# Performance work log

Hardware: AMD Instinct MI355X
Metric: run time of the kernel (lower is better)

Reference implementation:

```python
import jax, jax.numpy as jnp
import numpy as np
from jax import lax

B, C, H, W = 8, 384, 32, 32
HEADS, GROUPS = 12, 3
CG = C // GROUPS          # 128 channels per offset group
HD = C // HEADS           # 32 head dim
NS = H * W                # sampled kv points (one per query location)
EPS = 1e-5


def setup_inputs() -> dict:
    key = jax.random.key(0)
    ks = jax.random.split(key, 10)
    w = lambda k, sh, sc=0.02: (jax.random.normal(k, sh, jnp.float32) * sc)
    return {
        "x1": jax.random.normal(ks[0], (B, C, H, W), jnp.float32),
        "x2": jax.random.normal(ks[1], (B, C, H, W), jnp.float32),
        "Wq": w(ks[2], (C, C)), "bq": jnp.zeros((C,), jnp.float32),
        "Wk": w(ks[3], (C, C)), "bk": jnp.zeros((C,), jnp.float32),
        "Wv": w(ks[4], (C, C)), "bv": jnp.zeros((C,), jnp.float32),
        "Wo": w(ks[5], (C, C)), "bo": jnp.zeros((C,), jnp.float32),
        "off_dw": w(ks[6], (CG, 1, 5, 5)),       # depthwise 5x5 offset conv
        "off_dw_b": jnp.zeros((CG,), jnp.float32),
        "ln_g": jnp.ones((CG,), jnp.float32),
        "ln_b": jnp.zeros((CG,), jnp.float32),
        "off_w": w(ks[7], (2, CG), 0.01),         # 1x1 conv -> 2 offset channels
    }


def _conv1x1(x, Wm, bm):
    return jnp.einsum('oc,bchw->bohw', Wm, x) + bm[None, :, None, None]


def _ref_grid():
    # normalized reference points in [-1,1], channel 0 = x (width), 1 = y (height)
    xs = (jnp.arange(W, dtype=jnp.float32) + 0.5) / W * 2.0 - 1.0
    ys = (jnp.arange(H, dtype=jnp.float32) + 0.5) / H * 2.0 - 1.0
    gy, gx = jnp.meshgrid(ys, xs, indexing='ij')   # [H,W]
    return jnp.stack([gx, gy], axis=0)             # [2,H,W]


def _forward(x1, x2, Wq, bq, Wk, bk, Wv, bv, Wo, bo,
             off_dw, off_dw_b, ln_g, ln_b, off_w):
    BG = B * GROUPS
    q = _conv1x1(x1, Wq, bq)                                   # [B,C,H,W]

    # --- offset network (per group) ---
    qg = q.reshape(BG, CG, H, W)
    t = lax.conv_general_dilated(qg, off_dw, (1, 1), 'SAME',
                                 dimension_numbers=('NCHW', 'OIHW', 'NCHW'),
                                 feature_group_count=CG)
    t = t + off_dw_b[None, :, None, None]
    mu = jnp.mean(t, axis=1, keepdims=True)
    var = jnp.var(t, axis=1, keepdims=True)
    t = (t - mu) * lax.rsqrt(var + EPS)
    t = t * ln_g[None, :, None, None] + ln_b[None, :, None, None]
    t = jax.nn.gelu(t)
    off = jnp.einsum('oc,bchw->bohw', off_w, t)                # [BG,2,H,W]

    pos = jnp.clip(off + _ref_grid()[None], -1.0, 1.0)         # [BG,2,H,W]
    px = pos[:, 0].reshape(BG, NS)
    py = pos[:, 1].reshape(BG, NS)

    # --- bilinear grid_sample of x2 (align_corners=True) ---
    ix = (px + 1.0) * 0.5 * (W - 1)
    iy = (py + 1.0) * 0.5 * (H - 1)
    x0f, y0f = jnp.floor(ix), jnp.floor(iy)
    wx, wy = ix - x0f, iy - y0f
    x0 = jnp.clip(x0f.astype(jnp.int32), 0, W - 1)
    x1i = jnp.clip(x0 + 1, 0, W - 1)
    y0 = jnp.clip(y0f.astype(jnp.int32), 0, H - 1)
    y1i = jnp.clip(y0 + 1, 0, H - 1)

    x2g = x2.reshape(BG, CG, H * W)

    def gather(yi, xi):
        idx = yi * W + xi                                      # [BG,NS]
        idx = jnp.broadcast_to(idx[:, None, :], (BG, CG, NS))
        return jnp.take_along_axis(x2g, idx, axis=2)           # [BG,CG,NS]

    v00, v01 = gather(y0, x0), gather(y0, x1i)
    v10, v11 = gather(y1i, x0), gather(y1i, x1i)
    wx_, wy_ = wx[:, None, :], wy[:, None, :]
    samp = (v00 * (1 - wx_) * (1 - wy_) + v01 * wx_ * (1 - wy_)
            + v10 * (1 - wx_) * wy_ + v11 * wx_ * wy_)         # [BG,CG,NS]
    samp = samp.reshape(B, C, NS)

    # --- multi-head attention between q and sampled k/v ---
    k = jnp.einsum('oc,bcn->bon', Wk, samp) + bk[None, :, None]
    v = jnp.einsum('oc,bcn->bon', Wv, samp) + bv[None, :, None]
    qf = q.reshape(B, HEADS, HD, NS)
    kf = k.reshape(B, HEADS, HD, NS)
    vf = v.reshape(B, HEADS, HD, NS)
    scale = 1.0 / np.sqrt(HD).astype(np.float32)
    attn = jax.nn.softmax(jnp.einsum('bhdq,bhdk->bhqk', qf * scale, kf), axis=-1)
    out = jnp.einsum('bhqk,bhdk->bhdq', attn, vf).reshape(B, C, H, W)
    y = _conv1x1(out, Wo, bo)
    return x1 + y                                              # residual add (drop_path=0 -> Identity)


def reference(x1, x2, Wq, bq, Wk, bk, Wv, bv, Wo, bo,
              off_dw, off_dw_b, ln_g, ln_b, off_w):
    return _forward(x1, x2, Wq, bq, Wk, bk, Wv, bv, Wo, bo,
                    off_dw, off_dw_b, ln_g, ln_b, off_w)
```

## Files before the change

kernel.cpp:

```cpp
#include <hip/hip_runtime.h>
#include <math.h>

#define B_  8
#define C_  384
#define NS_ 1024
#define HEADS_ 12
#define HD_ 32
#define GROUPS_ 3
#define CG_ 128
#define EPS_ 1e-5f
#define QSC2 (0.17677669529663687f * 1.4426950408889634f)

typedef __attribute__((ext_vector_type(8))) short bf16x8;
typedef __attribute__((ext_vector_type(4))) short bf16x4;
typedef __attribute__((ext_vector_type(4))) float f32x4;
typedef __attribute__((ext_vector_type(8))) __bf16 b8;

static __device__ __forceinline__ short f2b(float f) {
  union { float f; unsigned u; } v; v.f = f;
  unsigned r = v.u + 0x7fffu + ((v.u >> 16) & 1u);
  return (short)(r >> 16);
}
static __device__ __forceinline__ float b2f(short s) {
  union { unsigned u; float f; } v; v.u = ((unsigned)(unsigned short)s) << 16;
  return v.f;
}

#if __has_builtin(__builtin_amdgcn_exp2f)
#define EXP2(x) __builtin_amdgcn_exp2f(x)
#else
#define EXP2(x) exp2f(x)
#endif

static __device__ __forceinline__ unsigned cvtpk(float lo, float hi) {
  unsigned r;
  asm("v_cvt_pk_bf16_f32 %0, %1, %2" : "=v"(r) : "v"(lo), "v"(hi));
  return r;
}

static __device__ __forceinline__ f32x4 MFMA(bf16x8 a, bf16x8 b, f32x4 c) {
  return __builtin_amdgcn_mfma_f32_16x16x32_bf16(
      __builtin_bit_cast(b8, a), __builtin_bit_cast(b8, b), c, 0, 0, 0);
}

__global__ void convw(const float* __restrict__ s0, const float* __restrict__ s1,
                      const float* __restrict__ s2, const float* __restrict__ s3,
                      short* __restrict__ d0, short* __restrict__ d1,
                      short* __restrict__ d2, short* __restrict__ d3, int n) {
  int i = blockIdx.x * 256 + threadIdx.x;
  if (i >= n) return;
  const float* s = blockIdx.y == 0 ? s0 : blockIdx.y == 1 ? s1 : blockIdx.y == 2 ? s2 : s3;
  short*       d = blockIdx.y == 0 ? d0 : blockIdx.y == 1 ? d1 : blockIdx.y == 2 ? d2 : d3;
  d[i] = f2b(s[i]);
}

__global__ void convdw(const float* __restrict__ dw, float* __restrict__ dwp) {
  int i = blockIdx.x * 256 + threadIdx.x;
  if (i < 25 * CG_) {
    int t = i / CG_, c = i % CG_;
    dwp[i] = dw[c * 25 + t];
  }
}

template <int CH>
__global__ __launch_bounds__(256) void transp(const float* __restrict__ src,
                                              short* __restrict__ dst) {
  __shared__ float tl[32][33];
  int n0 = blockIdx.x * 32, c0 = blockIdx.y * 32, b = blockIdx.z;
  int tx = threadIdx.x & 31, ty = threadIdx.x >> 5;
#pragma unroll
  for (int i = 0; i < 4; ++i)
    tl[ty + 8 * i][tx] = src[((size_t)b * CH + c0 + ty + 8 * i) * NS_ + n0 + tx];
  __syncthreads();
#pragma unroll
  for (int i = 0; i < 4; ++i)
    dst[((size_t)b * NS_ + n0 + ty + 8 * i) * CH + c0 + tx] = f2b(tl[tx][ty + 8 * i]);
}

#define GLOADA(kc_, AF)                                                        \
  _Pragma("unroll")                                                            \
  for (int rt = 0; rt < 4; ++rt)                                               \
    AF[rt] = *(const bf16x8*)(Ab + (size_t)(n0 + wr + rt * 16 + r15) * C_ +    \
                              (kc_) + g * 8);
#define GLOADB(kc_, BF, WP, MOFF)                                              \
  _Pragma("unroll")                                                            \
  for (int ct = 0; ct < 4; ++ct)                                               \
    BF[ct] = *(const bf16x8*)((WP) + (size_t)((MOFF) + ct * 16 + r15) * C_ +   \
                              (kc_) + g * 8);
#define GMFMA(AF, BF)                                                          \
  _Pragma("unroll")                                                            \
  for (int rt = 0; rt < 4; ++rt)                                               \
    _Pragma("unroll")                                                          \
    for (int ct = 0; ct < 4; ++ct) acc[rt][ct] = MFMA(AF[rt], BF[ct], acc[rt][ct]);

template <int MODE>
__global__ __launch_bounds__(256) void gemm_nm(
    const short* __restrict__ A, const short* __restrict__ Wb,
    const float* __restrict__ bias, const float* __restrict__ res,
    short* __restrict__ outb, float* __restrict__ outf) {
  int b = blockIdx.z;
  int n0 = blockIdx.x * 128;
  int m0 = blockIdx.y * 128;
  int wv = threadIdx.x >> 6;
  int lane = threadIdx.x & 63;
  int g = lane >> 4, r15 = lane & 15;
  int wr = (wv >> 1) * 64, wc = (wv & 1) * 64;

  const short* Ab = A + (size_t)b * NS_ * C_;
  f32x4 acc[4][4];
#pragma unroll
  for (int i = 0; i < 4; ++i)
#pragma unroll
    for (int j = 0; j < 4; ++j) acc[i][j] = (f32x4){0.f, 0.f, 0.f, 0.f};

  bf16x8 afA[4], bfA[4], afB[4], bfB[4];
  GLOADA(0, afA); GLOADB(0, bfA, Wb, m0 + wc);
#pragma unroll
  for (int cp = 0; cp < 6; ++cp) {
    GLOADA(64 * cp + 32, afB); GLOADB(64 * cp + 32, bfB, Wb, m0 + wc);
    GMFMA(afA, bfA);
    if (cp < 5) { GLOADA(64 * cp + 64, afA); GLOADB(64 * cp + 64, bfA, Wb, m0 + wc); }
    GMFMA(afB, bfB);
  }

#pragma unroll
  for (int rt = 0; rt < 4; ++rt)
#pragma unroll
    for (int ct = 0; ct < 4; ++ct) {
      int m = m0 + wc + ct * 16 + r15;
      int nb = n0 + wr + rt * 16 + g * 4;
      float bv = bias[m];
      f32x4 v = acc[rt][ct];
      v.x += bv; v.y += bv; v.z += bv; v.w += bv;
      if (MODE == 1) {
        *(f32x4*)(outf + ((size_t)b * C_ + m) * NS_ + nb) = v;
        outb[((size_t)b * NS_ + nb + 0) * C_ + m] = f2b(v.x * QSC2);
        outb[((size_t)b * NS_ + nb + 1) * C_ + m] = f2b(v.y * QSC2);
        outb[((size_t)b * NS_ + nb + 2) * C_ + m] = f2b(v.z * QSC2);
        outb[((size_t)b * NS_ + nb + 3) * C_ + m] = f2b(v.w * QSC2);
      } else {
        const f32x4 rv = *(const f32x4*)(res + ((size_t)b * C_ + m) * NS_ + nb);
        v.x += rv.x; v.y += rv.y; v.z += rv.z; v.w += rv.w;
        *(f32x4*)(outf + ((size_t)b * C_ + m) * NS_ + nb) = v;
      }
    }
}

__global__ __launch_bounds__(256) void gemm_kv(
    const short* __restrict__ A, const short* __restrict__ Wkb,
    const short* __restrict__ Wvb, const float* __restrict__ bkv,
    const float* __restrict__ bvv, short* __restrict__ kblk,
    short* __restrict__ vblk) {
  int b = blockIdx.z;
  int n0 = blockIdx.x * 128;
  int m0 = blockIdx.y * 64;
  int wv = threadIdx.x >> 6;
  int lane = threadIdx.x & 63;
  int g = lane >> 4, r15 = lane & 15;
  int wr = (wv >> 1) * 64;
  int isv = wv & 1;
  const short* Wsel = isv ? Wvb : Wkb;
  const float* bsel = isv ? bvv : bkv;

  const short* Ab = A + (size_t)b * NS_ * C_;
  f32x4 acc[4][4];
#pragma unroll
  for (int i = 0; i < 4; ++i)
#pragma unroll
    for (int j = 0; j < 4; ++j) acc[i][j] = (f32x4){0.f, 0.f, 0.f, 0.f};

  bf16x8 afA[4], bfA[4], afB[4], bfB[4];
  GLOADA(0, afA); GLOADB(0, bfA, Wsel, m0);
#pragma unroll
  for (int cp = 0; cp < 6; ++cp) {
    GLOADA(64 * cp + 32, afB); GLOADB(64 * cp + 32, bfB, Wsel, m0);
    GMFMA(afA, bfA);
    if (cp < 5) { GLOADA(64 * cp + 64, afA); GLOADB(64 * cp + 64, bfA, Wsel, m0); }
    GMFMA(afB, bfB);
  }

#pragma unroll
  for (int rt = 0; rt < 4; ++rt)
#pragma unroll
    for (int ct = 0; ct < 4; ++ct) {
      int m = m0 + ct * 16 + r15;
      int nb = n0 + wr + rt * 16 + g * 4;
      float bv = bsel[m];
      f32x4 v = acc[rt][ct];
      v.x += bv; v.y += bv; v.z += bv; v.w += bv;
      int h = m >> 5, dh = m & 31;
      if (!isv) {
        size_t hb = ((size_t)(b * HEADS_ + h) * 32 + (nb >> 5)) * 1024 +
                    (((nb >> 4) & 1) ? 512 : 0);
        int base_l = (nb & 15) | ((dh >> 3) << 4);
        int jj = dh & 7;
        kblk[hb + (size_t)(base_l + 0) * 8 + jj] = f2b(v.x);
        kblk[hb + (size_t)(base_l + 1) * 8 + jj] = f2b(v.y);
        kblk[hb + (size_t)(base_l + 2) * 8 + jj] = f2b(v.z);
        kblk[hb + (size_t)(base_l + 3) * 8 + jj] = f2b(v.w);
      } else {
        int dt = dh >> 4, q15v = dh & 15;
        int kk = nb & 31;
        int half = kk >> 4, gk = (kk & 15) >> 2;
        size_t off = ((size_t)(b * HEADS_ + h) * 32 + (nb >> 5)) * 1024 +
                     dt * 512 + (size_t)((q15v | (gk << 4))) * 8 + half * 4;
        bf16x4 s4 = {f2b(v.x), f2b(v.y), f2b(v.z), f2b(v.w)};
        *(bf16x4*)(vblk + off) = s4;
      }
    }
}

__global__ __launch_bounds__(256) void offsample4(
    const float* __restrict__ qd,
    const short* __restrict__ x2t,
    const float* __restrict__ dwp,
    const float* __restrict__ dwb,
    const float* __restrict__ lng, const float* __restrict__ lnb,
    const float* __restrict__ offw, short* __restrict__ samp) {
  int bg = blockIdx.x, y = blockIdx.y;
  int tid = threadIdx.x;
  int xg = tid >> 5, cc = tid & 31;
  int x0 = xg << 2, c0 = cc << 2;

  const float* qb = qd + ((size_t)bg * CG_ + c0) * NS_;

  f32x4 dwb4 = *(const f32x4*)(dwb + c0);
  float a[4][4];
#pragma unroll
  for (int i = 0; i < 4; ++i)
#pragma unroll
    for (int p = 0; p < 4; ++p) a[i][p] = dwb4[i];

#pragma unroll
  for (int dy = -2; dy <= 2; ++dy) {
    int yy = y + dy;
    if (yy < 0 || yy > 31) continue;
    f32x4 w0 = *(const f32x4*)(dwp + ((dy + 2) * 5 + 0) * CG_ + c0);
    f32x4 w1 = *(const f32x4*)(dwp + ((dy + 2) * 5 + 1) * CG_ + c0);
    f32x4 w2 = *(const f32x4*)(dwp + ((dy + 2) * 5 + 2) * CG_ + c0);
    f32x4 w3 = *(const f32x4*)(dwp + ((dy + 2) * 5 + 3) * CG_ + c0);
    f32x4 w4 = *(const f32x4*)(dwp + ((dy + 2) * 5 + 4) * CG_ + c0);
#pragma unroll
    for (int i = 0; i < 4; ++i) {
      const float* row = qb + (size_t)i * NS_ + yy * 32;
      f32x4 wa = (f32x4){0.f, 0.f, 0.f, 0.f};
      f32x4 wcv = (f32x4){0.f, 0.f, 0.f, 0.f};
      if (x0 >= 4)  wa  = *(const f32x4*)(row + x0 - 4);
      f32x4 wb = *(const f32x4*)(row + x0);
      if (x0 <= 24) wcv = *(const f32x4*)(row + x0 + 4);
      float w[12] = {wa[0], wa[1], wa[2], wa[3], wb[0], wb[1], wb[2], wb[3],
                     wcv[0], wcv[1], wcv[2], wcv[3]};
      float wt[5] = {w0[i], w1[i], w2[i], w3[i], w4[i]};
#pragma unroll
      for (int p = 0; p < 4; ++p)
#pragma unroll
        for (int j = 0; j < 5; ++j)
          a[i][p] = fmaf(w[p + j + 2], wt[j], a[i][p]);
    }
  }

  f32x4 sum = (f32x4){0.f, 0.f, 0.f, 0.f}, sumsq = sum;
#pragma unroll
  for (int i = 0; i < 4; ++i)
#pragma unroll
    for (int p = 0; p < 4; ++p) { sum[p] += a[i][p]; sumsq[p] += a[i][p] * a[i][p]; }
#pragma unroll
  for (int m = 1; m <= 16; m <<= 1) {
#pragma unroll
    for (int p = 0; p < 4; ++p) {
      sum[p]   += __shfl_xor(sum[p], m);
      sumsq[p] += __shfl_xor(sumsq[p], m);
    }
  }
  f32x4 mu, rs;
#pragma unroll
  for (int p = 0; p < 4; ++p) {
    mu[p] = sum[p] * (1.f / CG_);
    float var = sumsq[p] * (1.f / CG_) - mu[p] * mu[p];
    rs[p] = rsqrtf(var + EPS_);
  }

  f32x4 lg = *(const f32x4*)(lng + c0);
  f32x4 lb = *(const f32x4*)(lnb + c0);
  f32x4 ow0 = *(const f32x4*)(offw + c0);
  f32x4 ow1 = *(const f32x4*)(offw + CG_ + c0);
  f32x4 o0 = (f32x4){0.f, 0.f, 0.f, 0.f}, o1 = o0;
#pragma unroll
  for (int i = 0; i < 4; ++i)
#pragma unroll
    for (int p = 0; p < 4; ++p) {
      float z = (a[i][p] - mu[p]) * rs[p] * lg[i] + lb[i];
      float u = z * fmaf(0.044715f * z, z, 1.f);
      float e = __expf(-1.5957691216057308f * u);
      float ge = z * __builtin_amdgcn_rcpf(1.f + e);
      o0[p] = fmaf(ow0[i], ge, o0[p]);
      o1[p] = fmaf(ow1[i], ge, o1[p]);
    }
#pragma unroll
  for (int m = 1; m <= 16; m <<= 1) {
#pragma unroll
    for (int p = 0; p < 4; ++p) {
      o0[p] += __shfl_xor(o0[p], m);
      o1[p] += __shfl_xor(o1[p], m);
    }
  }

  int b = bg / GROUPS_, gi = bg % GROUPS_;
  const short* xb = x2t + (size_t)bg * NS_ * CG_ + c0;
  float gy = (y + 0.5f) * 0.0625f - 1.f;
#pragma unroll
  for (int p = 0; p < 4; ++p) {
    int x = x0 + p, n = y * 32 + x;
    float gx = (x + 0.5f) * 0.0625f - 1.f;
    float px = fminf(fmaxf(o0[p] + gx, -1.f), 1.f);
    float py = fminf(fmaxf(o1[p] + gy, -1.f), 1.f);
    float ix = (px + 1.f) * 0.5f * 31.f;
    float iy = (py + 1.f) * 0.5f * 31.f;
    float x0f = floorf(ix), y0f = floorf(iy);
    float wx = ix - x0f, wy = iy - y0f;
    int xa = min(max((int)x0f, 0), 31), xbb = min(xa + 1, 31);
    int ya = min(max((int)y0f, 0), 31), yb = min(ya + 1, 31);
    int i00 = ya * 32 + xa, i01 = ya * 32 + xbb;
    int i10 = yb * 32 + xa, i11 = yb * 32 + xbb;
    float w00 = (1.f - wx) * (1.f - wy), w01 = wx * (1.f - wy);
    float w10 = (1.f - wx) * wy,         w11 = wx * wy;
    bf16x4 v00 = *(const bf16x4*)(xb + (size_t)i00 * CG_);
    bf16x4 v01 = *(const bf16x4*)(xb + (size_t)i01 * CG_);
    bf16x4 v10 = *(const bf16x4*)(xb + (size_t)i10 * CG_);
    bf16x4 v11 = *(const bf16x4*)(xb + (size_t)i11 * CG_);
    short out4[4];
#pragma unroll
    for (int j = 0; j < 4; ++j) {
      float v = w00 * b2f(v00[j]) + w01 * b2f(v01[j]) +
                w10 * b2f(v10[j]) + w11 * b2f(v11[j]);
      out4[j] = f2b(v);
    }
    *(bf16x4*)(samp + ((size_t)b * NS_ + n) * C_ + gi * CG_ + c0) = *(bf16x4*)out4;
  }
}

__global__ __launch_bounds__(256) void attn_blk(
    const short* __restrict__ qn, const short* __restrict__ kblk,
    const short* __restrict__ vblk, short* __restrict__ op0,
    short* __restrict__ op1, float* __restrict__ lp) {
  int L = blockIdx.x;
  int tq = L >> 3;
  int task = (L & 7) + ((tq % 24) << 3);
  int qblk = tq / 24;
  int bh = task >> 1, s = task & 1;
  int b = bh / HEADS_, h = bh % HEADS_;
  int wv = threadIdx.x >> 6, lane = threadIdx.x & 63;
  int g = lane >> 4, q15 = lane & 15;
  int q0 = qblk * 128 + wv * 32;

  const short* Qb = qn + (size_t)b * NS_ * C_ + h * HD_;
  const short* Kc = kblk + ((size_t)(b * HEADS_ + h) * 32 + s * 16) * 1024 + lane * 8;
  const short* Vc = vblk + ((size_t)(b * HEADS_ + h) * 32 + s * 16) * 1024 + lane * 8;

  bf16x8 qf[2];
  qf[0] = *(const bf16x8*)(Qb + (size_t)(q0 + q15) * C_ + g * 8);
  qf[1] = *(const bf16x8*)(Qb + (size_t)(q0 + 16 + q15) * C_ + g * 8);

  f32x4 o[2][2];
  o[0][0] = o[0][1] = o[1][0] = o[1][1] = (f32x4){0.f, 0.f, 0.f, 0.f};
  f32x4 lv[2];
  lv[0] = lv[1] = (f32x4){0.f, 0.f, 0.f, 0.f};

#define LOADC(c_, K0, K1, V0, V1)                                              \
  {                                                                            \
    K0 = *(const bf16x8*)(Kc + (c_) * 1024);                                   \
    K1 = *(const bf16x8*)(Kc + (c_) * 1024 + 512);                             \
    V0 = *(const bf16x8*)(Vc + (c_) * 1024);                                   \
    V1 = *(const bf16x8*)(Vc + (c_) * 1024 + 512);                             \
  }

#define COMPUTEC(K0, K1, V0, V1)                                               \
  {                                                                            \
    _Pragma("unroll")                                                          \
    for (int qt = 0; qt < 2; ++qt) {                                           \
      f32x4 z_ = {0.f, 0.f, 0.f, 0.f};                                         \
      f32x4 t0 = MFMA(K0, qf[qt], z_);                                         \
      f32x4 t1 = MFMA(K1, qf[qt], z_);                                         \
      f32x4 e0, e1;                                                            \
      e0.x = EXP2(t0.x); e0.y = EXP2(t0.y); e0.z = EXP2(t0.z); e0.w = EXP2(t0.w);\
      e1.x = EXP2(t1.x); e1.y = EXP2(t1.y); e1.z = EXP2(t1.z); e1.w = EXP2(t1.w);\
      lv[qt] += e0; lv[qt] += e1;                                              \
      union { unsigned u[4]; bf16x8 v; } pu;                                   \
      pu.u[0] = cvtpk(e0.x, e0.y);                                             \
      pu.u[1] = cvtpk(e0.z, e0.w);                                             \
      pu.u[2] = cvtpk(e1.x, e1.y);                                             \
      pu.u[3] = cvtpk(e1.z, e1.w);                                             \
      o[qt][0] = MFMA(V0, pu.v, o[qt][0]);                                     \
      o[qt][1] = MFMA(V1, pu.v, o[qt][1]);                                     \
    }                                                                          \
  }

  bf16x8 kA0, kA1, vA0, vA1, kB0, kB1, vB0, vB1;
  LOADC(0, kA0, kA1, vA0, vA1);
#pragma unroll
  for (int cp = 0; cp < 8; ++cp) {
    LOADC(2 * cp + 1, kB0, kB1, vB0, vB1);
    COMPUTEC(kA0, kA1, vA0, vA1);
    if (cp < 7) LOADC(2 * cp + 2, kA0, kA1, vA0, vA1);
    COMPUTEC(kB0, kB1, vB0, vB1);
  }
#undef LOADC
#undef COMPUTEC

  short* opS = s ? op1 : op0;
#pragma unroll
  for (int qt = 0; qt < 2; ++qt) {
    float lt = (lv[qt].x + lv[qt].y) + (lv[qt].z + lv[qt].w);
    lt += __shfl_xor(lt, 16);
    lt += __shfl_xor(lt, 32);
    int q = q0 + qt * 16 + q15;
    if (g == 0) lp[((size_t)(s * B_ + b) * HEADS_ + h) * NS_ + q] = lt;
#pragma unroll
    for (int dt = 0; dt < 2; ++dt) {
      f32x4 ov = o[qt][dt];
      bf16x4 s4 = {f2b(ov.x), f2b(ov.y), f2b(ov.z), f2b(ov.w)};
      *(bf16x4*)(opS + ((size_t)b * NS_ + q) * C_ + h * HD_ + dt * 16 + g * 4) = s4;
    }
  }
}

__global__ __launch_bounds__(256) void attn_merge(
    const short* __restrict__ op0, const short* __restrict__ op1,
    const float* __restrict__ lp, short* __restrict__ on) {
  int idx = blockIdx.x * 256 + threadIdx.x;
  int c8 = idx % (C_ / 8);
  int q  = (idx / (C_ / 8)) % NS_;
  int b  = idx / ((C_ / 8) * NS_);
  int c0 = c8 * 8, h = c0 >> 5;
  size_t off = ((size_t)b * NS_ + q) * C_ + c0;
  bf16x8 a  = *(const bf16x8*)(op0 + off);
  bf16x8 bb = *(const bf16x8*)(op1 + off);
  float l = lp[((size_t)b * HEADS_ + h) * NS_ + q] +
            lp[((size_t)(B_ + b) * HEADS_ + h) * NS_ + q];
  float rl = 1.f / l;
  short r[8];
#pragma unroll
  for (int j = 0; j < 8; ++j) r[j] = f2b((b2f(a[j]) + b2f(bb[j])) * rl);
  *(bf16x8*)(on + off) = *(bf16x8*)r;
}

extern "C" void kernel_launch(void* const* d_in, const int* in_sizes, int n_in,
                              void* d_out, int out_size, void* d_ws, size_t ws_size,
                              hipStream_t stream) {
  const float* x1      = (const float*)d_in[0];
  const float* x2      = (const float*)d_in[1];
  const float* Wq      = (const float*)d_in[2];
  const float* bq      = (const float*)d_in[3];
  const float* Wk      = (const float*)d_in[4];
  const float* bk      = (const float*)d_in[5];
  const float* Wv      = (const float*)d_in[6];
  const float* bv      = (const float*)d_in[7];
  const float* Wo      = (const float*)d_in[8];
  const float* bo      = (const float*)d_in[9];
  const float* off_dw  = (const float*)d_in[10];
  const float* off_dwb = (const float*)d_in[11];
  const float* ln_g    = (const float*)d_in[12];
  const float* ln_b    = (const float*)d_in[13];
  const float* off_w   = (const float*)d_in[14];

  char* base = (char*)d_ws;
  const size_t SZ = (size_t)B_ * C_ * NS_;
  float* q_dC  = (float*)base;
  short* q_nC  = (short*)(base + SZ * 4);
  short* samp  = (short*)(base + SZ * 6);
  short* k_blk = (short*)(base + SZ * 8);
  short* v_blk = (short*)(base + SZ * 10);
  short* o_nC  = (short*)(base + SZ * 12);
  short* x1t   = (short*)(base + SZ * 14);
  short* Wqb   = (short*)(base + SZ * 16);
  short* Wkb   = Wqb + C_ * C_;
  short* Wvb   = Wkb + C_ * C_;
  short* Wob   = Wvb + C_ * C_;
  short* x2t   = (short*)(base + SZ * 18);
  float* dwp   = (float*)(base + SZ * 20);
  short* op0   = samp;
  short* op1   = x1t;
  float* lp    = q_dC;

  dim3 gg(NS_ / 128, C_ / 128, B_);

  convw<<<dim3((C_ * C_ + 255) / 256, 4), 256, 0, stream>>>(
      Wq, Wk, Wv, Wo, Wqb, Wkb, Wvb, Wob, C_ * C_);
  convdw<<<dim3(13), 256, 0, stream>>>(off_dw, dwp);
  transp<C_><<<dim3(NS_ / 32, C_ / 32, B_), 256, 0, stream>>>(x1, x1t);
  transp<CG_><<<dim3(NS_ / 32, CG_ / 32, B_ * GROUPS_), 256, 0, stream>>>(x2, x2t);
  gemm_nm<1><<<gg, 256, 0, stream>>>(x1t, Wqb, bq, nullptr, q_nC, q_dC);
  offsample4<<<dim3(B_ * GROUPS_, 32), 256, 0, stream>>>(
      q_dC, x2t, dwp, off_dwb, ln_g, ln_b, off_w, samp);
  gemm_kv<<<dim3(NS_ / 128, C_ / 64, B_), 256, 0, stream>>>(
      samp, Wkb, Wvb, bk, bv, k_blk, v_blk);
  attn_blk<<<dim3(1536), 256, 0, stream>>>(q_nC, k_blk, v_blk, op0, op1, lp);
  attn_merge<<<dim3(B_ * NS_ * (C_ / 8) / 256), 256, 0, stream>>>(op0, op1, lp, o_nC);
  gemm_nm<3><<<gg, 256, 0, stream>>>(o_nC, Wob, bo, x1, nullptr, (float*)d_out);
}
```

Before: 139.8 us.

## Merge prep kernels into one launch and drop split-KV attention merge

Folds the four preprocessing kernels (weight bf16 conversion, depthwise weight permute, x1/x2 transposes) into a single prep launch dispatched by block index. Attention no longer splits the KV range in two; each block walks all 32 KV chunks and normalizes by the row sum in-register, which removes the attn_merge kernel and its round trip of partial outputs and sums through memory. The trade-off is half as many attention blocks (768 instead of 1536), each with a loop twice as long, so there is less parallelism on the device.

```diff
diff --git a/kernel.cpp b/kernel.cpp
--- a/kernel.cpp
+++ b/kernel.cpp
@@ -43,38 +43,51 @@
       __builtin_bit_cast(b8, a), __builtin_bit_cast(b8, b), c, 0, 0, 0);
 }
 
-__global__ void convw(const float* __restrict__ s0, const float* __restrict__ s1,
-                      const float* __restrict__ s2, const float* __restrict__ s3,
-                      short* __restrict__ d0, short* __restrict__ d1,
-                      short* __restrict__ d2, short* __restrict__ d3, int n) {
-  int i = blockIdx.x * 256 + threadIdx.x;
-  if (i >= n) return;
-  const float* s = blockIdx.y == 0 ? s0 : blockIdx.y == 1 ? s1 : blockIdx.y == 2 ? s2 : s3;
-  short*       d = blockIdx.y == 0 ? d0 : blockIdx.y == 1 ? d1 : blockIdx.y == 2 ? d2 : d3;
-  d[i] = f2b(s[i]);
-}
-
-__global__ void convdw(const float* __restrict__ dw, float* __restrict__ dwp) {
-  int i = blockIdx.x * 256 + threadIdx.x;
-  if (i < 25 * CG_) {
-    int t = i / CG_, c = i % CG_;
-    dwp[i] = dw[c * 25 + t];
-  }
-}
-
-template <int CH>
-__global__ __launch_bounds__(256) void transp(const float* __restrict__ src,
-                                              short* __restrict__ dst) {
+__global__ __launch_bounds__(256) void prep(
+    const float* __restrict__ x1, const float* __restrict__ x2,
+    const float* __restrict__ Wq, const float* __restrict__ Wk,
+    const float* __restrict__ Wv, const float* __restrict__ Wo,
+    const float* __restrict__ dw,
+    short* __restrict__ x1t, short* __restrict__ x2t,
+    short* __restrict__ Wqb, short* __restrict__ Wkb,
+    short* __restrict__ Wvb, short* __restrict__ Wob,
+    float* __restrict__ dwp) {
   __shared__ float tl[32][33];
-  int n0 = blockIdx.x * 32, c0 = blockIdx.y * 32, b = blockIdx.z;
-  int tx = threadIdx.x & 31, ty = threadIdx.x >> 5;
-#pragma unroll
-  for (int i = 0; i < 4; ++i)
-    tl[ty + 8 * i][tx] = src[((size_t)b * CH + c0 + ty + 8 * i) * NS_ + n0 + tx];
-  __syncthreads();
-#pragma unroll
-  for (int i = 0; i < 4; ++i)
-    dst[((size_t)b * NS_ + n0 + ty + 8 * i) * CH + c0 + tx] = f2b(tl[tx][ty + 8 * i]);
+  int id = blockIdx.x;
+  int tid = threadIdx.x;
+  int tx = tid & 31, ty = tid >> 5;
+  if (id < 3072) {
+    int nb = id & 31, cb = (id >> 5) % 12, b = id / 384;
+    int n0 = nb * 32, c0 = cb * 32;
+#pragma unroll
+    for (int i = 0; i < 4; ++i)
+      tl[ty + 8 * i][tx] = x1[((size_t)b * C_ + c0 + ty + 8 * i) * NS_ + n0 + tx];
+    __syncthreads();
+#pragma unroll
+    for (int i = 0; i < 4; ++i)
+      x1t[((size_t)b * NS_ + n0 + ty + 8 * i) * C_ + c0 + tx] = f2b(tl[tx][ty + 8 * i]);
+  } else if (id < 6144) {
+    int i = id - 3072;
+    int nb = i & 31, cb = (i >> 5) & 3, bg = i / 128;
+    int n0 = nb * 32, c0 = cb * 32;
+#pragma unroll
+    for (int j = 0; j < 4; ++j)
+      tl[ty + 8 * j][tx] = x2[((size_t)bg * CG_ + c0 + ty + 8 * j) * NS_ + n0 + tx];
+    __syncthreads();
+#pragma unroll
+    for (int j = 0; j < 4; ++j)
+      x2t[((size_t)bg * NS_ + n0 + ty + 8 * j) * CG_ + c0 + tx] = f2b(tl[tx][ty + 8 * j]);
+  } else if (id < 8448) {
+    int i = id - 6144;
+    int mat = i / 576;
+    int e = (i % 576) * 256 + tid;
+    const float* s = mat == 0 ? Wq : mat == 1 ? Wk : mat == 2 ? Wv : Wo;
+    short*       d = mat == 0 ? Wqb : mat == 1 ? Wkb : mat == 2 ? Wvb : Wob;
+    d[e] = f2b(s[e]);
+  } else {
+    int e = (id - 8448) * 256 + tid;
+    if (e < 25 * CG_) { int t = e / CG_, c = e % CG_; dwp[e] = dw[c * 25 + t]; }
+  }
 }
 
 #define GLOADA(kc_, AF)                                                        \
@@ -211,10 +224,8 @@
 }
 
 __global__ __launch_bounds__(256) void offsample4(
-    const float* __restrict__ qd,
-    const short* __restrict__ x2t,
-    const float* __restrict__ dwp,
-    const float* __restrict__ dwb,
+    const float* __restrict__ qd, const short* __restrict__ x2t,
+    const float* __restrict__ dwp, const float* __restrict__ dwb,
     const float* __restrict__ lng, const float* __restrict__ lnb,
     const float* __restrict__ offw, short* __restrict__ samp) {
   int bg = blockIdx.x, y = blockIdx.y;
@@ -341,21 +352,19 @@
 
 __global__ __launch_bounds__(256) void attn_blk(
     const short* __restrict__ qn, const short* __restrict__ kblk,
-    const short* __restrict__ vblk, short* __restrict__ op0,
-    short* __restrict__ op1, float* __restrict__ lp) {
+    const short* __restrict__ vblk, short* __restrict__ on) {
   int L = blockIdx.x;
   int tq = L >> 3;
-  int task = (L & 7) + ((tq % 24) << 3);
-  int qblk = tq / 24;
-  int bh = task >> 1, s = task & 1;
+  int bh = (L & 7) + ((tq % 12) << 3);
+  int qblk = tq / 12;
   int b = bh / HEADS_, h = bh % HEADS_;
   int wv = threadIdx.x >> 6, lane = threadIdx.x & 63;
   int g = lane >> 4, q15 = lane & 15;
   int q0 = qblk * 128 + wv * 32;
 
   const short* Qb = qn + (size_t)b * NS_ * C_ + h * HD_;
-  const short* Kc = kblk + ((size_t)(b * HEADS_ + h) * 32 + s * 16) * 1024 + lane * 8;
-  const short* Vc = vblk + ((size_t)(b * HEADS_ + h) * 32 + s * 16) * 1024 + lane * 8;
+  const short* Kc = kblk + (size_t)(b * HEADS_ + h) * 32768 + lane * 8;
+  const short* Vc = vblk + (size_t)(b * HEADS_ + h) * 32768 + lane * 8;
 
   bf16x8 qf[2];
   qf[0] = *(const bf16x8*)(Qb + (size_t)(q0 + q15) * C_ + g * 8);
@@ -398,50 +407,29 @@
   bf16x8 kA0, kA1, vA0, vA1, kB0, kB1, vB0, vB1;
   LOADC(0, kA0, kA1, vA0, vA1);
 #pragma unroll
-  for (int cp = 0; cp < 8; ++cp) {
+  for (int cp = 0; cp < 16; ++cp) {
     LOADC(2 * cp + 1, kB0, kB1, vB0, vB1);
     COMPUTEC(kA0, kA1, vA0, vA1);
-    if (cp < 7) LOADC(2 * cp + 2, kA0, kA1, vA0, vA1);
+    if (cp < 15) LOADC(2 * cp + 2, kA0, kA1, vA0, vA1);
     COMPUTEC(kB0, kB1, vB0, vB1);
   }
 #undef LOADC
 #undef COMPUTEC
 
-  short* opS = s ? op1 : op0;
 #pragma unroll
   for (int qt = 0; qt < 2; ++qt) {
     float lt = (lv[qt].x + lv[qt].y) + (lv[qt].z + lv[qt].w);
     lt += __shfl_xor(lt, 16);
     lt += __shfl_xor(lt, 32);
+    float rl = 1.f / lt;
     int q = q0 + qt * 16 + q15;
-    if (g == 0) lp[((size_t)(s * B_ + b) * HEADS_ + h) * NS_ + q] = lt;
 #pragma unroll
     for (int dt = 0; dt < 2; ++dt) {
       f32x4 ov = o[qt][dt];
-      bf16x4 s4 = {f2b(ov.x), f2b(ov.y), f2b(ov.z), f2b(ov.w)};
-      *(bf16x4*)(opS + ((size_t)b * NS_ + q) * C_ + h * HD_ + dt * 16 + g * 4) = s4;
-    }
-  }
-}
-
-__global__ __launch_bounds__(256) void attn_merge(
-    const short* __restrict__ op0, const short* __restrict__ op1,
-    const float* __restrict__ lp, short* __restrict__ on) {
-  int idx = blockIdx.x * 256 + threadIdx.x;
-  int c8 = idx % (C_ / 8);
-  int q  = (idx / (C_ / 8)) % NS_;
-  int b  = idx / ((C_ / 8) * NS_);
-  int c0 = c8 * 8, h = c0 >> 5;
-  size_t off = ((size_t)b * NS_ + q) * C_ + c0;
-  bf16x8 a  = *(const bf16x8*)(op0 + off);
-  bf16x8 bb = *(const bf16x8*)(op1 + off);
-  float l = lp[((size_t)b * HEADS_ + h) * NS_ + q] +
-            lp[((size_t)(B_ + b) * HEADS_ + h) * NS_ + q];
-  float rl = 1.f / l;
-  short r[8];
-#pragma unroll
-  for (int j = 0; j < 8; ++j) r[j] = f2b((b2f(a[j]) + b2f(bb[j])) * rl);
-  *(bf16x8*)(on + off) = *(bf16x8*)r;
+      bf16x4 s4 = {f2b(ov.x * rl), f2b(ov.y * rl), f2b(ov.z * rl), f2b(ov.w * rl)};
+      *(bf16x4*)(on + ((size_t)b * NS_ + q) * C_ + h * HD_ + dt * 16 + g * 4) = s4;
+    }
+  }
 }
 
 extern "C" void kernel_launch(void* const* d_in, const int* in_sizes, int n_in,
@@ -472,29 +460,22 @@
   short* v_blk = (short*)(base + SZ * 10);
   short* o_nC  = (short*)(base + SZ * 12);
   short* x1t   = (short*)(base + SZ * 14);
-  short* Wqb   = (short*)(base + SZ * 16);
+  short* x2t   = (short*)(base + SZ * 16);
+  short* Wqb   = (short*)(base + SZ * 18);
   short* Wkb   = Wqb + C_ * C_;
   short* Wvb   = Wkb + C_ * C_;
   short* Wob   = Wvb + C_ * C_;
-  short* x2t   = (short*)(base + SZ * 18);
-  float* dwp   = (float*)(base + SZ * 20);
-  short* op0   = samp;
-  short* op1   = x1t;
-  float* lp    = q_dC;
+  float* dwp   = (float*)(base + SZ * 18 + (size_t)8 * C_ * C_);
 
   dim3 gg(NS_ / 128, C_ / 128, B_);
 
-  convw<<<dim3((C_ * C_ + 255) / 256, 4), 256, 0, stream>>>(
-      Wq, Wk, Wv, Wo, Wqb, Wkb, Wvb, Wob, C_ * C_);
-  convdw<<<dim3(13), 256, 0, stream>>>(off_dw, dwp);
-  transp<C_><<<dim3(NS_ / 32, C_ / 32, B_), 256, 0, stream>>>(x1, x1t);
-  transp<CG_><<<dim3(NS_ / 32, CG_ / 32, B_ * GROUPS_), 256, 0, stream>>>(x2, x2t);
+  prep<<<dim3(8461), 256, 0, stream>>>(x1, x2, Wq, Wk, Wv, Wo, off_dw,
+                                       x1t, x2t, Wqb, Wkb, Wvb, Wob, dwp);
   gemm_nm<1><<<gg, 256, 0, stream>>>(x1t, Wqb, bq, nullptr, q_nC, q_dC);
   offsample4<<<dim3(B_ * GROUPS_, 32), 256, 0, stream>>>(
       q_dC, x2t, dwp, off_dwb, ln_g, ln_b, off_w, samp);
   gemm_kv<<<dim3(NS_ / 128, C_ / 64, B_), 256, 0, stream>>>(
       samp, Wkb, Wvb, bk, bv, k_blk, v_blk);
-  attn_blk<<<dim3(1536), 256, 0, stream>>>(q_nC, k_blk, v_blk, op0, op1, lp);
-  attn_merge<<<dim3(B_ * NS_ * (C_ / 8) / 256), 256, 0, stream>>>(op0, op1, lp, o_nC);
+  attn_blk<<<dim3(768), 256, 0, stream>>>(q_nC, k_blk, v_blk, o_nC);
   gemm_nm<3><<<gg, 256, 0, stream>>>(o_nC, Wob, bo, x1, nullptr, (float*)d_out);
 }
```

After: 175.3 us. +25.4%, slower.
